# Performance work log

Measured on AMD Instinct MI355X. Metric: run time of the kernel, lower is better.

## Reference

```python
import jax, jax.numpy as jnp
import numpy as np

B, N, D, H, C = 1, 256, 128, 4, 32
EPS = 1e-5

def setup_inputs() -> dict:
    key = jax.random.key(0)
    ks = jax.random.split(key, 10)
    s = 1.0 / np.sqrt(D)
    return {
        "Z_raw": jax.random.normal(ks[0], (B, N, N, D), dtype=jnp.float32),
        "Z_mask": jnp.ones((B, N, N), dtype=jnp.float32),
        "ln_w": jnp.ones((D,), dtype=jnp.float32),
        "ln_b": jnp.zeros((D,), dtype=jnp.float32),
        "b_proj_w": (jax.random.normal(ks[1], (H, D), dtype=jnp.float32) * s),
        "wq": jax.random.normal(ks[2], (D, H * C), dtype=jnp.float32) * s,
        "wk": jax.random.normal(ks[3], (D, H * C), dtype=jnp.float32) * s,
        "wv": jax.random.normal(ks[4], (D, H * C), dtype=jnp.float32) * s,
        "wg": jax.random.normal(ks[5], (D, H * C), dtype=jnp.float32) * s,
        "bg": jnp.ones((H * C,), dtype=jnp.float32),  # FastFold inits gating bias to 1
        "wo": jax.random.normal(ks[6], (H * C, D), dtype=jnp.float32) / np.sqrt(H * C),
        "out_bias": jnp.zeros((D,), dtype=jnp.float32),
    }

def reference(Z_raw, Z_mask, ln_w, ln_b, b_proj_w, wq, wk, wv, wg, bg, wo, out_bias):
    # LayerNorm over d_pair
    mu = jnp.mean(Z_raw, axis=-1, keepdims=True)
    var = jnp.mean(jnp.square(Z_raw - mu), axis=-1, keepdims=True)
    Z = (Z_raw - mu) * jax.lax.rsqrt(var + EPS) * ln_w + ln_b  # [B,N,N,D]

    # Triangle bias: b[b,h,q,k] (shared across rows i)
    tb = jnp.einsum('bqkd,hd->bhqk', Z, b_proj_w)  # [B,H,N,N]

    scale = 1.0 / np.sqrt(C)
    q = jnp.einsum('bijd,de->bije', Z, wq).reshape(B, N, N, H, C) * scale
    k = jnp.einsum('bijd,de->bije', Z, wk).reshape(B, N, N, H, C)
    v = jnp.einsum('bijd,de->bije', Z, wv).reshape(B, N, N, H, C)

    logits = jnp.einsum('biqhc,bikhc->bihqk', q, k)  # [B,I,H,N,N]
    mask_bias = 1e9 * (Z_mask - 1.0)  # [B,I,J]
    logits = logits + mask_bias[:, :, None, None, :] + tb[:, None]
    attn = jax.nn.softmax(logits, axis=-1)

    o = jnp.einsum('bihqk,bikhc->biqhc', attn, v)  # [B,I,N,H,C]
    gate = jax.nn.sigmoid(jnp.einsum('bijd,de->bije', Z, wg) + bg)
    o = o.reshape(B, N, N, H * C) * gate
    out = jnp.einsum('bije,ed->bijd', o, wo)

    # bias_dropout_add (eval mode: dropout is identity; dropout_mask is ones)
    return Z_raw + out + out_bias
```

## Files before the change

kernel.cpp:

```cpp
#include <hip/hip_runtime.h>
#include <hip/hip_bf16.h>


#define NN 256
#define DD 128
#define NP (NN*NN)

typedef __hip_bfloat16 bf16;
typedef unsigned short u16;
typedef unsigned int u32;
typedef __bf16 bf16x8 __attribute__((ext_vector_type(8)));
typedef short s16x4 __attribute__((ext_vector_type(4)));
typedef float f32x4 __attribute__((ext_vector_type(4)));

__device__ __forceinline__ float b2f(bf16 x) { return __bfloat162float(x); }
__device__ __forceinline__ bf16 f2b(float x) { return __float2bfloat16(x); }
__device__ __forceinline__ float lo16(u32 u) { return __uint_as_float(u << 16); }
__device__ __forceinline__ float hi16(u32 u) { return __uint_as_float(u & 0xFFFF0000u); }
__device__ __forceinline__ float fexp2(float x) { return __builtin_amdgcn_exp2f(x); }
__device__ __forceinline__ bool bf16_mode(const void* lnw_raw) {
    return ((const u32*)lnw_raw)[0] == 0x3F803F80u;
}
__device__ __forceinline__ u32 pk2(float a, float b) {
    union { bf16 h; u16 u; } ca, cb; ca.h = f2b(a); cb.h = f2b(b);
    return ((u32)cb.u << 16) | (u32)ca.u;
}
__device__ __forceinline__ bf16x8 ld_frag(const u32* p) {
    uint4 r = *(const uint4*)p;
    return __builtin_bit_cast(bf16x8, r);
}
#define MFMA16(a,b,c) __builtin_amdgcn_mfma_f32_16x16x32_bf16(a,b,c,0,0,0)
#define MFMA16K(a,b,c) __builtin_amdgcn_mfma_f32_16x16x16bf16_1k(a,b,c,0,0,0)
#define PLANE(et) (((size_t)(et)) << 19)

#define OFF_ZM    0
#define OFF_LNW   65536
#define OFF_LNB   65664
#define OFF_BPW   65792
#define OFF_WQ    66304
#define OFF_WK    82688
#define OFF_WV    99072
#define OFF_WG    115456
#define OFF_BG    131840
#define OFF_WO    131968
#define OFF_OBIAS 148352
#define CANON_TOTAL 148480
#define OFF_WQT   148480
#define OFF_WKT   164864
#define OFF_WVT   181248
#define OFF_WGT   197632
#define OFF_WOT   214016
#define CANONT_TOTAL 81920

#define SCALE 0.17677669529663687f
#define LOG2E 1.4426950408889634f

__global__ __launch_bounds__(256) void k_conv(
    const void* zm, const void* lnw, const void* lnb, const void* bpw,
    const void* wq, const void* wk, const void* wv, const void* wg,
    const void* bg, const void* wo, const void* obias, bf16* canon)
{
    const bool bfm = bf16_mode(lnw);
    int idx = blockIdx.x * 256 + threadIdx.x;
    if (idx >= CANON_TOTAL) return;
    const void* src; int off;
    if      (idx < OFF_LNW)   { src = zm;    off = idx; }
    else if (idx < OFF_LNB)   { src = lnw;   off = idx - OFF_LNW; }
    else if (idx < OFF_BPW)   { src = lnb;   off = idx - OFF_LNB; }
    else if (idx < OFF_WQ)    { src = bpw;   off = idx - OFF_BPW; }
    else if (idx < OFF_WK)    { src = wq;    off = idx - OFF_WQ; }
    else if (idx < OFF_WV)    { src = wk;    off = idx - OFF_WK; }
    else if (idx < OFF_WG)    { src = wv;    off = idx - OFF_WV; }
    else if (idx < OFF_BG)    { src = wg;    off = idx - OFF_WG; }
    else if (idx < OFF_WO)    { src = bg;    off = idx - OFF_BG; }
    else if (idx < OFF_OBIAS) { src = wo;    off = idx - OFF_WO; }
    else                      { src = obias; off = idx - OFF_OBIAS; }
    float f = bfm ? b2f(((const bf16*)src)[off]) : ((const float*)src)[off];
    if (idx >= OFF_BPW && idx < OFF_WQ) f *= LOG2E;
    if (idx >= OFF_BG  && idx < OFF_WO) f *= LOG2E;
    canon[idx] = f2b(f);
}

__global__ __launch_bounds__(256) void k_convT(bf16* canon)
{
    int idx = blockIdx.x * 256 + threadIdx.x;
    if (idx >= CANONT_TOTAL) return;
    int m = idx >> 14, r = idx & 16383;
    int a = r >> 7, b = r & 127;
    int src = (m==0) ? OFF_WQ : (m==1) ? OFF_WK : (m==2) ? OFF_WV
            : (m==3) ? OFF_WG : OFF_WO;
    float v = b2f(canon[src + b*128 + a]);
    if (m == 0) v *= SCALE*LOG2E;
    if (m == 3) v *= LOG2E;
    canon[OFF_WQT + idx] = f2b(v);
}

__global__ __launch_bounds__(256, 3) void k_ln_qkv(
    const void* __restrict__ Zr, const void* __restrict__ lnw_raw,
    const bf16* __restrict__ canon,
    u32* __restrict__ znw, u32* __restrict__ qbw, u32* __restrict__ kbw,
    u32* __restrict__ vbTw, float* __restrict__ tbw)
{
    __shared__ u32 zs[64*68];
    const bool bfm = bf16_mode(lnw_raw);
    const u32* cw = (const u32*)canon;
    const int t = threadIdx.x;
    const int base = blockIdx.x * 64;
    const int p = t >> 2, l = t & 3;
    const int pair = base + p;

    float vals[32];
    if (bfm) {
        const u32* zr = (const u32*)Zr + (size_t)pair*64 + l*16;
        #pragma unroll
        for (int j = 0; j < 16; ++j) {
            u32 u = zr[j];
            vals[2*j] = lo16(u); vals[2*j+1] = hi16(u);
        }
    } else {
        const float* zr = (const float*)Zr + (size_t)pair*128 + l*32;
        #pragma unroll
        for (int j = 0; j < 32; ++j) vals[j] = zr[j];
    }

    float s = 0.f;
    #pragma unroll
    for (int m = 0; m < 32; ++m) s += vals[m];
    s += __shfl_xor(s, 1); s += __shfl_xor(s, 2);
    const float mu = s * (1.f/128.f);
    float s2 = 0.f;
    #pragma unroll
    for (int m = 0; m < 32; ++m) { float d = vals[m] - mu; s2 += d*d; }
    s2 += __shfl_xor(s2, 1); s2 += __shfl_xor(s2, 2);
    const float rstd = rsqrtf(s2 * (1.f/128.f) + 1e-5f);

    const u32* lnw_w = cw + (OFF_LNW>>1) + l*16;
    const u32* lnb_w = cw + (OFF_LNB>>1) + l*16;
    #pragma unroll
    for (int j = 0; j < 16; ++j) {
        u32 uw = lnw_w[j], ub = lnb_w[j];
        float z0 = (vals[2*j]  -mu)*rstd*lo16(uw) + lo16(ub);
        float z1 = (vals[2*j+1]-mu)*rstd*hi16(uw) + hi16(ub);
        zs[p*68 + l*16 + j] = pk2(z0, z1);
    }
    __syncthreads();

    #pragma unroll
    for (int j = 0; j < 16; ++j) {
        int idx = j*256 + t;
        znw[(size_t)base*64 + idx] = zs[(idx>>6)*68 + (idx&63)];
    }

    const int wv_ = t >> 6, lane = t & 63, qn = lane & 15, quad = lane >> 4;

    {
        f32x4 dtb = {0.f,0.f,0.f,0.f};
        #pragma unroll
        for (int ks = 0; ks < 4; ++ks) {
            bf16x8 a = ld_frag(cw + (OFF_BPW>>1) + qn*64 + ks*16 + quad*4);
            bf16x8 zbq = ld_frag(&zs[(wv_*16+qn)*68 + ks*16 + quad*4]);
            dtb = MFMA16(a, zbq, dtb);
        }
        if (quad == 0) {
            const int pc = base + wv_*16 + qn;
            tbw[0*NP + pc] = dtb[0];
            tbw[1*NP + pc] = dtb[1];
            tbw[2*NP + pc] = dtb[2];
            tbw[3*NP + pc] = dtb[3];
        }
    }

    const int ib = base >> 8;
    const int jbase = (base & 255);

    #pragma unroll
    for (int ei = 0; ei < 2; ++ei) {
        const int et = wv_*2 + ei;
        bf16x8 aq[4], ak[4], av[4];
        #pragma unroll
        for (int ks = 0; ks < 4; ++ks) {
            aq[ks] = ld_frag(cw + (OFF_WQT>>1) + (et*16+qn)*64 + ks*16 + quad*4);
            ak[ks] = ld_frag(cw + (OFF_WKT>>1) + (et*16+qn)*64 + ks*16 + quad*4);
            av[ks] = ld_frag(cw + (OFF_WVT>>1) + (et*16+qn)*64 + ks*16 + quad*4);
        }
        const int e = et*16 + qn;
        u32* vrow = vbTw + (size_t)((ib*4 + (e>>5))*32 + (e&31))*128;
        #pragma unroll
        for (int pg = 0; pg < 4; ++pg) {
            bf16x8 zb[4];
            #pragma unroll
            for (int ks = 0; ks < 4; ++ks)
                zb[ks] = ld_frag(&zs[(pg*16+qn)*68 + ks*16 + quad*4]);
            f32x4 dq = {0.f,0.f,0.f,0.f}, dk = {0.f,0.f,0.f,0.f}, dv = {0.f,0.f,0.f,0.f};
            #pragma unroll
            for (int ks = 0; ks < 4; ++ks) {
                dq = MFMA16(aq[ks], zb[ks], dq);
                dk = MFMA16(ak[ks], zb[ks], dk);
                dv = MFMA16(zb[ks], av[ks], dv);
            }
            const size_t pr = (size_t)(base + pg*16 + qn)*8 + quad*2;
            uint2 sq; sq.x = pk2(dq[0], dq[1]); sq.y = pk2(dq[2], dq[3]);
            *(uint2*)(qbw + PLANE(et) + pr) = sq;
            uint2 sk; sk.x = pk2(dk[0], dk[1]); sk.y = pk2(dk[2], dk[3]);
            *(uint2*)(kbw + PLANE(et) + pr) = sk;
            const int jj = jbase + pg*16 + quad*4;
            uint2 sv2; sv2.x = pk2(dv[0], dv[1]); sv2.y = pk2(dv[2], dv[3]);
            *(uint2*)(vrow + (jj>>1)) = sv2;
        }
    }
}

__global__ __launch_bounds__(256, 3) void k_attn(
    const u32* __restrict__ qb, const u32* __restrict__ kb,
    const u32* __restrict__ vbT, const bf16* __restrict__ canon,
    const float* __restrict__ tbw, u32* __restrict__ ob)
{
    __shared__ u32 ks_s[256*16];
    __shared__ u32 vs_s[32*128];
    __shared__ float mb_s[256];
    const int t = threadIdx.x;
    const int i = blockIdx.x & 255, h = blockIdx.x >> 8;

    {
        const uint4* kp0 = (const uint4*)(kb + PLANE(2*h)   + (size_t)i*2048);
        const uint4* kp1 = (const uint4*)(kb + PLANE(2*h+1) + (size_t)i*2048);
        #pragma unroll
        for (int r = 0; r < 2; ++r) {
            int q4 = t + 256*r;
            int p = q4 >> 1;
            int c0 = (q4 & 1);
            int c1 = 2 + (q4 & 1);
            uint4 a = kp0[q4];
            *(uint4*)&ks_s[p*16 + ((c0 + (p>>1)) & 3)*4] = a;
            uint4 b = kp1[q4];
            *(uint4*)&ks_s[p*16 + ((c1 + (p>>1)) & 3)*4] = b;
        }
    }
    #pragma unroll
    for (int r = 0; r < 4; ++r) {
        int u = t + 256*r;
        int row = u >> 5, d4 = (u & 31)*4;
        *(uint4*)&vs_s[row*128 + (d4 ^ ((row & 7) << 2))] =
            *(const uint4*)(vbT + (size_t)((i*4+h)*32 + row)*128 + d4);
    }
    {
        u32 w = ((const u32*)canon)[(OFF_ZM>>1) + i*128 + (t>>1)];
        float m = (t & 1) ? hi16(w) : lo16(w);
        mb_s[t] = 1.4426950e9f * (m - 1.f);
    }
    __syncthreads();

    const int wave = t >> 6, lane = t & 63;
    const int qn = lane & 15, quad = lane >> 4;
    const int ksw = ((quad + (qn>>1)) & 3) * 4;
    const int vswz = (qn & 7) << 2;

    for (int qt = 0; qt < 4; ++qt) {
        const int qg = wave*64 + qt*16 + qn;
        const float* tbq = tbw + h*NP + qg*256 + quad*4;
        bf16x8 qf = ld_frag(qb + PLANE(2*h + (quad>>1)) + (size_t)(i*256+qg)*8 + (quad&1)*4);

        float sum = 0.f;
        f32x4 o0 = {0.f,0.f,0.f,0.f}, o1 = {0.f,0.f,0.f,0.f};

        #pragma unroll
        for (int half = 0; half < 2; ++half) {
            f32x4 sv8[8];
            #pragma unroll
            for (int kk = 0; kk < 8; ++kk) {
                const int kt = half*8 + kk;
                f32x4 mb4 = *(const f32x4*)&mb_s[kt*16 + quad*4];
                sv8[kk] = *(const f32x4*)(tbq + kt*16) + mb4;
            }
            #pragma unroll
            for (int kk = 0; kk < 8; ++kk) {
                const int kt = half*8 + kk;
                bf16x8 kf = ld_frag(&ks_s[(kt*16+qn)*16 + ksw]);
                sv8[kk] = MFMA16(kf, qf, sv8[kk]);
            }

            #pragma unroll
            for (int kk = 0; kk < 8; ++kk) {
                const int kt = half*8 + kk;
                float e0 = fexp2(sv8[kk][0]);
                float e1 = fexp2(sv8[kk][1]);
                float e2 = fexp2(sv8[kk][2]);
                float e3 = fexp2(sv8[kk][3]);
                sum += (e0 + e1) + (e2 + e3);
                uint2 pw2; pw2.x = pk2(e0, e1); pw2.y = pk2(e2, e3);
                s16x4 pf = __builtin_bit_cast(s16x4, pw2);
                const int vcol = (kt*8 + quad*2) ^ vswz;
                s16x4 v0 = __builtin_bit_cast(s16x4, *(const uint2*)&vs_s[qn*128 + vcol]);
                s16x4 v1 = __builtin_bit_cast(s16x4, *(const uint2*)&vs_s[(16+qn)*128 + vcol]);
                o0 = MFMA16K(v0, pf, o0);
                o1 = MFMA16K(v1, pf, o1);
                __builtin_amdgcn_sched_barrier(0);
            }
        }
        sum += __shfl_xor(sum, 16);
        sum += __shfl_xor(sum, 32);

        const float rinv = 1.f / sum;
        uint2 s0, s1;
        s0.x = pk2(o0[0]*rinv, o0[1]*rinv); s0.y = pk2(o0[2]*rinv, o0[3]*rinv);
        s1.x = pk2(o1[0]*rinv, o1[1]*rinv); s1.y = pk2(o1[2]*rinv, o1[3]*rinv);
        u32* opb = ob + PLANE(2*h) + (size_t)(i*256+qg)*8 + quad*2;
        *(uint2*)opb = s0;
        *(uint2*)(opb + (1u<<19)) = s1;
    }
}

__global__ __launch_bounds__(256, 3) void k_gateout(
    const void* __restrict__ Zr, const void* __restrict__ lnw_raw,
    const bf16* __restrict__ canon,
    const u32* __restrict__ znw, const u32* __restrict__ obw,
    void* __restrict__ outp)
{
    __shared__ u32 og_s[64*68];
    const bool bfm = bf16_mode(lnw_raw);
    const u32* cw = (const u32*)canon;
    const int t = threadIdx.x;
    const int base = blockIdx.x * 64;
    const int wv_ = t >> 6, lane = t & 63, qn = lane & 15, quad = lane >> 4;

    bf16x8 awg[2][4];
    uint2 bg2[2];
    #pragma unroll
    for (int ei = 0; ei < 2; ++ei) {
        const int et = wv_*2 + ei;
        #pragma unroll
        for (int ks = 0; ks < 4; ++ks)
            awg[ei][ks] = ld_frag(cw + (OFF_WGT>>1) + (et*16+qn)*64 + ks*16 + quad*4);
        bg2[ei] = *(const uint2*)(cw + (OFF_BG>>1) + et*8 + quad*2);
    }
    #pragma unroll
    for (int pg = 0; pg < 4; ++pg) {
        const size_t pair = base + pg*16 + qn;
        bf16x8 zb[4];
        #pragma unroll
        for (int ks = 0; ks < 4; ++ks)
            zb[ks] = ld_frag(znw + pair*64 + ks*16 + quad*4);
        #pragma unroll
        for (int ei = 0; ei < 2; ++ei) {
            const int et = wv_*2 + ei;
            f32x4 ag = {0.f,0.f,0.f,0.f};
            #pragma unroll
            for (int ks = 0; ks < 4; ++ks) ag = MFMA16(awg[ei][ks], zb[ks], ag);
            uint2 ob2 = *(const uint2*)(obw + PLANE(et) + pair*8 + quad*2);
            float r0 = lo16(ob2.x) / (1.f + fexp2(-(ag[0] + lo16(bg2[ei].x))));
            float r1 = hi16(ob2.x) / (1.f + fexp2(-(ag[1] + hi16(bg2[ei].x))));
            float r2 = lo16(ob2.y) / (1.f + fexp2(-(ag[2] + lo16(bg2[ei].y))));
            float r3 = hi16(ob2.y) / (1.f + fexp2(-(ag[3] + hi16(bg2[ei].y))));
            uint2 w; w.x = pk2(r0, r1); w.y = pk2(r2, r3);
            *(uint2*)&og_s[(pg*16+qn)*68 + et*8 + quad*2] = w;
        }
    }
    __syncthreads();

    bf16x8 awo[2][4];
    uint2 oi2[2];
    #pragma unroll
    for (int di = 0; di < 2; ++di) {
        const int dt = wv_*2 + di;
        #pragma unroll
        for (int ks = 0; ks < 4; ++ks)
            awo[di][ks] = ld_frag(cw + (OFF_WOT>>1) + (dt*16+qn)*64 + ks*16 + quad*4);
        oi2[di] = *(const uint2*)(cw + (OFF_OBIAS>>1) + dt*8 + quad*2);
    }
    #pragma unroll
    for (int pg = 0; pg < 4; ++pg) {
        const size_t pair = base + pg*16 + qn;
        const size_t prow = pair*64;
        bf16x8 ogb[4];
        #pragma unroll
        for (int ks = 0; ks < 4; ++ks)
            ogb[ks] = ld_frag(&og_s[(pg*16+qn)*68 + ks*16 + quad*4]);
        #pragma unroll
        for (int di = 0; di < 2; ++di) {
            const int dt = wv_*2 + di;
            f32x4 ao = {0.f,0.f,0.f,0.f};
            #pragma unroll
            for (int ks = 0; ks < 4; ++ks) ao = MFMA16(awo[di][ks], ogb[ks], ao);
            const float b0 = lo16(oi2[di].x), b1 = hi16(oi2[di].x);
            const float b2v = lo16(oi2[di].y), b3 = hi16(oi2[di].y);
            if (bfm) {
                uint2 zr2 = *(const uint2*)((const u32*)Zr + prow + dt*8 + quad*2);
                uint2 w;
                w.x = pk2(ao[0] + b0 + lo16(zr2.x), ao[1] + b1 + hi16(zr2.x));
                w.y = pk2(ao[2] + b2v + lo16(zr2.y), ao[3] + b3 + hi16(zr2.y));
                *(uint2*)((u32*)outp + prow + dt*8 + quad*2) = w;
            } else {
                const float* zr = (const float*)Zr + pair*128 + dt*16 + quad*4;
                float4 z4 = *(const float4*)zr;
                float4 w;
                w.x = ao[0] + b0 + z4.x;  w.y = ao[1] + b1 + z4.y;
                w.z = ao[2] + b2v + z4.z; w.w = ao[3] + b3 + z4.w;
                *(float4*)((float*)outp + pair*128 + dt*16 + quad*4) = w;
            }
        }
    }
}

extern "C" void kernel_launch(void* const* d_in, const int* in_sizes, int n_in,
                              void* d_out, int out_size, void* d_ws, size_t ws_size,
                              hipStream_t stream)
{
    const void* Zr    = d_in[0];
    const void* Zm    = d_in[1];
    const void* lnw   = d_in[2];
    const void* lnb   = d_in[3];
    const void* bpw   = d_in[4];
    const void* wq    = d_in[5];
    const void* wk    = d_in[6];
    const void* wv    = d_in[7];
    const void* wg    = d_in[8];
    const void* bg    = d_in[9];
    const void* wo    = d_in[10];
    const void* obias = d_in[11];

    char* ws = (char*)d_ws;
    const size_t M = 16777216;
    u32* znw   = (u32*)(ws);
    u32* qbw   = (u32*)(ws + 1*M);
    u32* kbw   = (u32*)(ws + 2*M);
    u32* vbTw  = (u32*)(ws + 3*M);
    u32* obw   = (u32*)(ws + 4*M);
    float* tbw = (float*)(ws + 5*M);
    bf16* canon = (bf16*)(ws + 5*M + 1048576);

    hipLaunchKernelGGL(k_conv, dim3((CANON_TOTAL+255)/256), dim3(256), 0, stream,
                       Zm, lnw, lnb, bpw, wq, wk, wv, wg, bg, wo, obias, canon);
    hipLaunchKernelGGL(k_convT, dim3((CANONT_TOTAL+255)/256), dim3(256), 0, stream,
                       canon);
    hipLaunchKernelGGL(k_ln_qkv, dim3(1024), dim3(256), 0, stream,
                       Zr, lnw, canon, znw, qbw, kbw, vbTw, tbw);
    hipLaunchKernelGGL(k_attn, dim3(1024), dim3(256), 0, stream,
                       qbw, kbw, vbTw, canon, tbw, obw);
    hipLaunchKernelGGL(k_gateout, dim3(1024), dim3(256), 0, stream,
                       Zr, lnw, canon, znw, obw, d_out);
}
```

Before: 184.9 us.

## Move gate projection into QKV kernel and apply gating inside attention

The gate projection and its sigmoid are now computed in the LN/QKV kernel, which already holds the normalized Z tile in shared memory. That kernel writes the gate as a bf16 plane, and the attention epilogue multiplies it into the normalized output. The normalized-Z write-out and the gate GEMM in the output kernel go away, and the output kernel reads gated O directly from planes without a shared-memory stage. The two weight conversion kernels are also merged into one launch that transposes straight from the raw inputs. The cost is extra MFMA work and register pressure in the QKV kernel, plus an extra gate read in attention.

```diff
diff --git a/kernel.cpp b/kernel.cpp
--- a/kernel.cpp
+++ b/kernel.cpp
@@ -62,44 +62,42 @@
 {
     const bool bfm = bf16_mode(lnw);
     int idx = blockIdx.x * 256 + threadIdx.x;
-    if (idx >= CANON_TOTAL) return;
-    const void* src; int off;
-    if      (idx < OFF_LNW)   { src = zm;    off = idx; }
-    else if (idx < OFF_LNB)   { src = lnw;   off = idx - OFF_LNW; }
-    else if (idx < OFF_BPW)   { src = lnb;   off = idx - OFF_LNB; }
-    else if (idx < OFF_WQ)    { src = bpw;   off = idx - OFF_BPW; }
-    else if (idx < OFF_WK)    { src = wq;    off = idx - OFF_WQ; }
-    else if (idx < OFF_WV)    { src = wk;    off = idx - OFF_WK; }
-    else if (idx < OFF_WG)    { src = wv;    off = idx - OFF_WV; }
-    else if (idx < OFF_BG)    { src = wg;    off = idx - OFF_WG; }
-    else if (idx < OFF_WO)    { src = bg;    off = idx - OFF_BG; }
-    else if (idx < OFF_OBIAS) { src = wo;    off = idx - OFF_WO; }
-    else                      { src = obias; off = idx - OFF_OBIAS; }
-    float f = bfm ? b2f(((const bf16*)src)[off]) : ((const float*)src)[off];
-    if (idx >= OFF_BPW && idx < OFF_WQ) f *= LOG2E;
-    if (idx >= OFF_BG  && idx < OFF_WO) f *= LOG2E;
-    canon[idx] = f2b(f);
-}
-
-__global__ __launch_bounds__(256) void k_convT(bf16* canon)
-{
-    int idx = blockIdx.x * 256 + threadIdx.x;
-    if (idx >= CANONT_TOTAL) return;
-    int m = idx >> 14, r = idx & 16383;
-    int a = r >> 7, b = r & 127;
-    int src = (m==0) ? OFF_WQ : (m==1) ? OFF_WK : (m==2) ? OFF_WV
-            : (m==3) ? OFF_WG : OFF_WO;
-    float v = b2f(canon[src + b*128 + a]);
-    if (m == 0) v *= SCALE*LOG2E;
-    if (m == 3) v *= LOG2E;
-    canon[OFF_WQT + idx] = f2b(v);
+    if (idx < CANON_TOTAL) {
+        const void* src; int off;
+        if      (idx < OFF_LNW)   { src = zm;    off = idx; }
+        else if (idx < OFF_LNB)   { src = lnw;   off = idx - OFF_LNW; }
+        else if (idx < OFF_BPW)   { src = lnb;   off = idx - OFF_LNB; }
+        else if (idx < OFF_WQ)    { src = bpw;   off = idx - OFF_BPW; }
+        else if (idx < OFF_WK)    { src = wq;    off = idx - OFF_WQ; }
+        else if (idx < OFF_WV)    { src = wk;    off = idx - OFF_WK; }
+        else if (idx < OFF_WG)    { src = wv;    off = idx - OFF_WV; }
+        else if (idx < OFF_BG)    { src = wg;    off = idx - OFF_WG; }
+        else if (idx < OFF_WO)    { src = bg;    off = idx - OFF_BG; }
+        else if (idx < OFF_OBIAS) { src = wo;    off = idx - OFF_WO; }
+        else                      { src = obias; off = idx - OFF_OBIAS; }
+        float f = bfm ? b2f(((const bf16*)src)[off]) : ((const float*)src)[off];
+        if (idx >= OFF_BPW && idx < OFF_WQ) f *= LOG2E;
+        if (idx >= OFF_BG  && idx < OFF_WO) f *= LOG2E;
+        canon[idx] = f2b(f);
+    } else if (idx < CANON_TOTAL + CANONT_TOTAL) {
+        int i2 = idx - CANON_TOTAL;
+        int m = i2 >> 14, r = i2 & 16383;
+        int a = r >> 7, b = r & 127;
+        const void* s = (m==0) ? wq : (m==1) ? wk : (m==2) ? wv
+                      : (m==3) ? wg : wo;
+        float v = bfm ? b2f(((const bf16*)s)[b*128 + a])
+                      : ((const float*)s)[b*128 + a];
+        if (m == 0) v *= SCALE*LOG2E;
+        if (m == 3) v *= LOG2E;
+        canon[OFF_WQT + i2] = f2b(v);
+    }
 }
 
 __global__ __launch_bounds__(256, 3) void k_ln_qkv(
     const void* __restrict__ Zr, const void* __restrict__ lnw_raw,
     const bf16* __restrict__ canon,
-    u32* __restrict__ znw, u32* __restrict__ qbw, u32* __restrict__ kbw,
-    u32* __restrict__ vbTw, float* __restrict__ tbw)
+    u32* __restrict__ qbw, u32* __restrict__ kbw,
+    u32* __restrict__ vbTw, u32* __restrict__ gbw, float* __restrict__ tbw)
 {
     __shared__ u32 zs[64*68];
     const bool bfm = bf16_mode(lnw_raw);
@@ -145,12 +143,6 @@
     }
     __syncthreads();
 
-    #pragma unroll
-    for (int j = 0; j < 16; ++j) {
-        int idx = j*256 + t;
-        znw[(size_t)base*64 + idx] = zs[(idx>>6)*68 + (idx&63)];
-    }
-
     const int wv_ = t >> 6, lane = t & 63, qn = lane & 15, quad = lane >> 4;
 
     {
@@ -176,13 +168,15 @@
     #pragma unroll
     for (int ei = 0; ei < 2; ++ei) {
         const int et = wv_*2 + ei;
-        bf16x8 aq[4], ak[4], av[4];
+        bf16x8 aq[4], ak[4], av[4], ag[4];
         #pragma unroll
         for (int ks = 0; ks < 4; ++ks) {
             aq[ks] = ld_frag(cw + (OFF_WQT>>1) + (et*16+qn)*64 + ks*16 + quad*4);
             ak[ks] = ld_frag(cw + (OFF_WKT>>1) + (et*16+qn)*64 + ks*16 + quad*4);
             av[ks] = ld_frag(cw + (OFF_WVT>>1) + (et*16+qn)*64 + ks*16 + quad*4);
-        }
+            ag[ks] = ld_frag(cw + (OFF_WGT>>1) + (et*16+qn)*64 + ks*16 + quad*4);
+        }
+        const uint2 bgv = *(const uint2*)(cw + (OFF_BG>>1) + et*8 + quad*2);
         const int e = et*16 + qn;
         u32* vrow = vbTw + (size_t)((ib*4 + (e>>5))*32 + (e&31))*128;
         #pragma unroll
@@ -191,18 +185,26 @@
             #pragma unroll
             for (int ks = 0; ks < 4; ++ks)
                 zb[ks] = ld_frag(&zs[(pg*16+qn)*68 + ks*16 + quad*4]);
-            f32x4 dq = {0.f,0.f,0.f,0.f}, dk = {0.f,0.f,0.f,0.f}, dv = {0.f,0.f,0.f,0.f};
+            f32x4 dq = {0.f,0.f,0.f,0.f}, dk = {0.f,0.f,0.f,0.f};
+            f32x4 dv = {0.f,0.f,0.f,0.f}, dg = {0.f,0.f,0.f,0.f};
             #pragma unroll
             for (int ks = 0; ks < 4; ++ks) {
                 dq = MFMA16(aq[ks], zb[ks], dq);
                 dk = MFMA16(ak[ks], zb[ks], dk);
                 dv = MFMA16(zb[ks], av[ks], dv);
+                dg = MFMA16(ag[ks], zb[ks], dg);
             }
             const size_t pr = (size_t)(base + pg*16 + qn)*8 + quad*2;
             uint2 sq; sq.x = pk2(dq[0], dq[1]); sq.y = pk2(dq[2], dq[3]);
             *(uint2*)(qbw + PLANE(et) + pr) = sq;
             uint2 sk; sk.x = pk2(dk[0], dk[1]); sk.y = pk2(dk[2], dk[3]);
             *(uint2*)(kbw + PLANE(et) + pr) = sk;
+            float g0 = 1.f / (1.f + fexp2(-(dg[0] + lo16(bgv.x))));
+            float g1 = 1.f / (1.f + fexp2(-(dg[1] + hi16(bgv.x))));
+            float g2 = 1.f / (1.f + fexp2(-(dg[2] + lo16(bgv.y))));
+            float g3 = 1.f / (1.f + fexp2(-(dg[3] + hi16(bgv.y))));
+            uint2 sg; sg.x = pk2(g0, g1); sg.y = pk2(g2, g3);
+            *(uint2*)(gbw + PLANE(et) + pr) = sg;
             const int jj = jbase + pg*16 + quad*4;
             uint2 sv2; sv2.x = pk2(dv[0], dv[1]); sv2.y = pk2(dv[2], dv[3]);
             *(uint2*)(vrow + (jj>>1)) = sv2;
@@ -213,7 +215,8 @@
 __global__ __launch_bounds__(256, 3) void k_attn(
     const u32* __restrict__ qb, const u32* __restrict__ kb,
     const u32* __restrict__ vbT, const bf16* __restrict__ canon,
-    const float* __restrict__ tbw, u32* __restrict__ ob)
+    const float* __restrict__ tbw, const u32* __restrict__ gb,
+    u32* __restrict__ ob)
 {
     __shared__ u32 ks_s[256*16];
     __shared__ u32 vs_s[32*128];
@@ -300,63 +303,32 @@
         sum += __shfl_xor(sum, 16);
         sum += __shfl_xor(sum, 32);
 
+        const u32* gpb = gb + PLANE(2*h) + (size_t)(i*256+qg)*8 + quad*2;
+        uint2 ga = *(const uint2*)gpb;
+        uint2 gc = *(const uint2*)(gpb + (1u<<19));
         const float rinv = 1.f / sum;
         uint2 s0, s1;
-        s0.x = pk2(o0[0]*rinv, o0[1]*rinv); s0.y = pk2(o0[2]*rinv, o0[3]*rinv);
-        s1.x = pk2(o1[0]*rinv, o1[1]*rinv); s1.y = pk2(o1[2]*rinv, o1[3]*rinv);
+        s0.x = pk2(o0[0]*rinv*lo16(ga.x), o0[1]*rinv*hi16(ga.x));
+        s0.y = pk2(o0[2]*rinv*lo16(ga.y), o0[3]*rinv*hi16(ga.y));
+        s1.x = pk2(o1[0]*rinv*lo16(gc.x), o1[1]*rinv*hi16(gc.x));
+        s1.y = pk2(o1[2]*rinv*lo16(gc.y), o1[3]*rinv*hi16(gc.y));
         u32* opb = ob + PLANE(2*h) + (size_t)(i*256+qg)*8 + quad*2;
         *(uint2*)opb = s0;
         *(uint2*)(opb + (1u<<19)) = s1;
     }
 }
 
-__global__ __launch_bounds__(256, 3) void k_gateout(
+__global__ __launch_bounds__(256, 3) void k_out(
     const void* __restrict__ Zr, const void* __restrict__ lnw_raw,
     const bf16* __restrict__ canon,
-    const u32* __restrict__ znw, const u32* __restrict__ obw,
-    void* __restrict__ outp)
+    const u32* __restrict__ obg, void* __restrict__ outp)
 {
-    __shared__ u32 og_s[64*68];
     const bool bfm = bf16_mode(lnw_raw);
     const u32* cw = (const u32*)canon;
     const int t = threadIdx.x;
     const int base = blockIdx.x * 64;
     const int wv_ = t >> 6, lane = t & 63, qn = lane & 15, quad = lane >> 4;
 
-    bf16x8 awg[2][4];
-    uint2 bg2[2];
-    #pragma unroll
-    for (int ei = 0; ei < 2; ++ei) {
-        const int et = wv_*2 + ei;
-        #pragma unroll
-        for (int ks = 0; ks < 4; ++ks)
-            awg[ei][ks] = ld_frag(cw + (OFF_WGT>>1) + (et*16+qn)*64 + ks*16 + quad*4);
-        bg2[ei] = *(const uint2*)(cw + (OFF_BG>>1) + et*8 + quad*2);
-    }
-    #pragma unroll
-    for (int pg = 0; pg < 4; ++pg) {
-        const size_t pair = base + pg*16 + qn;
-        bf16x8 zb[4];
-        #pragma unroll
-        for (int ks = 0; ks < 4; ++ks)
-            zb[ks] = ld_frag(znw + pair*64 + ks*16 + quad*4);
-        #pragma unroll
-        for (int ei = 0; ei < 2; ++ei) {
-            const int et = wv_*2 + ei;
-            f32x4 ag = {0.f,0.f,0.f,0.f};
-            #pragma unroll
-            for (int ks = 0; ks < 4; ++ks) ag = MFMA16(awg[ei][ks], zb[ks], ag);
-            uint2 ob2 = *(const uint2*)(obw + PLANE(et) + pair*8 + quad*2);
-            float r0 = lo16(ob2.x) / (1.f + fexp2(-(ag[0] + lo16(bg2[ei].x))));
-            float r1 = hi16(ob2.x) / (1.f + fexp2(-(ag[1] + hi16(bg2[ei].x))));
-            float r2 = lo16(ob2.y) / (1.f + fexp2(-(ag[2] + lo16(bg2[ei].y))));
-            float r3 = hi16(ob2.y) / (1.f + fexp2(-(ag[3] + hi16(bg2[ei].y))));
-            uint2 w; w.x = pk2(r0, r1); w.y = pk2(r2, r3);
-            *(uint2*)&og_s[(pg*16+qn)*68 + et*8 + quad*2] = w;
-        }
-    }
-    __syncthreads();
-
     bf16x8 awo[2][4];
     uint2 oi2[2];
     #pragma unroll
@@ -374,7 +346,7 @@
         bf16x8 ogb[4];
         #pragma unroll
         for (int ks = 0; ks < 4; ++ks)
-            ogb[ks] = ld_frag(&og_s[(pg*16+qn)*68 + ks*16 + quad*4]);
+            ogb[ks] = ld_frag(obg + PLANE(2*ks + (quad>>1)) + pair*8 + (quad&1)*4);
         #pragma unroll
         for (int di = 0; di < 2; ++di) {
             const int dt = wv_*2 + di;
@@ -420,7 +392,7 @@
 
     char* ws = (char*)d_ws;
     const size_t M = 16777216;
-    u32* znw   = (u32*)(ws);
+    u32* gbw   = (u32*)(ws);
     u32* qbw   = (u32*)(ws + 1*M);
     u32* kbw   = (u32*)(ws + 2*M);
     u32* vbTw  = (u32*)(ws + 3*M);
@@ -428,14 +400,13 @@
     float* tbw = (float*)(ws + 5*M);
     bf16* canon = (bf16*)(ws + 5*M + 1048576);
 
-    hipLaunchKernelGGL(k_conv, dim3((CANON_TOTAL+255)/256), dim3(256), 0, stream,
+    hipLaunchKernelGGL(k_conv, dim3((CANON_TOTAL+CANONT_TOTAL+255)/256), dim3(256),
+                       0, stream,
                        Zm, lnw, lnb, bpw, wq, wk, wv, wg, bg, wo, obias, canon);
-    hipLaunchKernelGGL(k_convT, dim3((CANONT_TOTAL+255)/256), dim3(256), 0, stream,
-                       canon);
     hipLaunchKernelGGL(k_ln_qkv, dim3(1024), dim3(256), 0, stream,
-                       Zr, lnw, canon, znw, qbw, kbw, vbTw, tbw);
+                       Zr, lnw, canon, qbw, kbw, vbTw, gbw, tbw);
     hipLaunchKernelGGL(k_attn, dim3(1024), dim3(256), 0, stream,
-                       qbw, kbw, vbTw, canon, tbw, obw);
-    hipLaunchKernelGGL(k_gateout, dim3(1024), dim3(256), 0, stream,
-                       Zr, lnw, canon, znw, obw, d_out);
-}
+                       qbw, kbw, vbTw, canon, tbw, gbw, obw);
+    hipLaunchKernelGGL(k_out, dim3(1024), dim3(256), 0, stream,
+                       Zr, lnw, canon, obw, d_out);
+}
```

Result: no change. 183.5 us (-0.7%).
